# Performance work log

Measured on AMD Instinct MI355X. Metric: run time of the kernel, lower is better.

Reference implementation:

```python
import math
import jax, jax.numpy as jnp
import numpy as np

T, B, E, H = 2048, 1, 2048, 32
HD = E // H          # head_dim = 64
HALF = HD // 2       # rotary half = 32
SCALE_LENGTH = 1024


def duplicate_interleave(m):
    # [S, HALF] -> [S, HD], each column duplicated adjacently
    return jnp.repeat(m, 2, axis=-1)


def rotate_every_two(x):
    # x: [BH, S, HD]
    x1 = x[:, :, ::2]
    x2 = x[:, :, 1::2]
    return jnp.stack((-x2, x1), axis=-1).reshape(x.shape)


def apply_rotary_pos_emb(x, sin, cos, scale):
    # sin/cos/scale: [S, HALF]; x: [BH, S, HD]
    sin2 = duplicate_interleave(sin * scale)
    cos2 = duplicate_interleave(cos * scale)
    return x * cos2 + rotate_every_two(x) * sin2


def setup_inputs() -> dict:
    key = jax.random.key(0)
    ks = jax.random.split(key, 8)
    std = 0.02
    query = jax.random.normal(ks[0], (T, B, E), jnp.float32)
    key_t = jax.random.normal(ks[1], (T, B, E), jnp.float32)
    value = jax.random.normal(ks[2], (T, B, E), jnp.float32)
    Wq = jax.random.normal(ks[3], (E, E), jnp.float32) * std
    Wk = jax.random.normal(ks[4], (E, E), jnp.float32) * std
    Wv = jax.random.normal(ks[5], (E, E), jnp.float32) * std
    Wo = jax.random.normal(ks[6], (E, E), jnp.float32) * std
    bq = jnp.zeros((E,), jnp.float32)
    bk = jnp.zeros((E,), jnp.float32)
    bv = jnp.zeros((E,), jnp.float32)
    bo = jnp.zeros((E,), jnp.float32)
    # XPos-style rotary tables
    pos = jnp.arange(T, dtype=jnp.float32)
    inv_freq = 1.0 / (10000.0 ** (jnp.arange(HALF, dtype=jnp.float32) / HALF))
    ang = pos[:, None] * inv_freq[None, :]          # [T, HALF]
    sin = jnp.sin(ang)
    cos = jnp.cos(ang)
    scale_base = 512.0
    dim_scale = (jnp.arange(0, HD, 2, dtype=jnp.float32) + 0.4 * HD) / (1.4 * HD)
    xscale = dim_scale[None, :] ** (pos[:, None] / scale_base)  # [T, HALF]
    # causal additive mask
    attn_mask = jnp.where(jnp.triu(jnp.ones((T, T), bool), k=1), -1e9, 0.0).astype(jnp.float32)
    return {"query": query, "key": key_t, "value": value,
            "Wq": Wq, "bq": bq, "Wk": Wk, "bk": bk, "Wv": Wv, "bv": bv,
            "Wo": Wo, "bo": bo, "sin": sin, "cos": cos, "xscale": xscale,
            "attn_mask": attn_mask, "scale_length": SCALE_LENGTH}


def reference(query, key, value, Wq, bq, Wk, bk, Wv, bv, Wo, bo,
              sin, cos, xscale, attn_mask, scale_length):
    tgt_len, bsz, embed_dim = query.shape
    scaling = HD ** -0.5

    def proj(x, W, b):
        y = x @ W.T + b                                # [T, B, E]
        return y.reshape(tgt_len, bsz * H, HD).transpose(1, 0, 2)  # [BH, T, HD]

    q = proj(query, Wq, bq)
    k = proj(key, Wk, bk)
    v = proj(value, Wv, bv)

    # self-attention XPos rotary: k scaled by 1/xscale, q by xscale (last q_len rows)
    k = apply_rotary_pos_emb(k, sin, cos, 1.0 / xscale)
    q = apply_rotary_pos_emb(q, sin[-tgt_len:], cos[-tgt_len:], xscale[-tgt_len:])

    src_len = k.shape[1]
    if src_len > scale_length:
        pos_k = jnp.arange(src_len - tgt_len, src_len, dtype=jnp.float32)
        scale_attention = jnp.maximum(1.0, jnp.log(pos_k) / math.log(scale_length))
        q = q * scale_attention[None, :, None]

    q = q * scaling
    attn_weights = jnp.einsum('btd,bsd->bts', q, k)      # [BH, T, S]
    attn_weights = attn_weights + attn_mask[None, :, :]
    attn_weights = jax.nn.softmax(attn_weights.astype(jnp.float32), axis=-1
                                  ).astype(q.dtype)
    attn = jnp.einsum('bts,bsd->btd', attn_weights, v)   # [BH, T, HD]
    attn = attn.transpose(1, 0, 2).reshape(tgt_len, bsz, embed_dim)
    attn = attn @ Wo.T + bo
    return attn
```

## Files before the change

### kernel.cpp

```cpp
#include <hip/hip_runtime.h>
#include <hip/hip_bf16.h>
#include <math.h>

#define T_LEN 2048
#define EMB   2048
#define NH    32
#define HD    64
#define HALF  32

typedef __attribute__((ext_vector_type(8))) short short8v;
typedef __attribute__((ext_vector_type(4))) float floatx4;

__device__ inline void gload_lds16(const void* g, void* l) {
    __builtin_amdgcn_global_load_lds(
        (const __attribute__((address_space(1))) unsigned int*)g,
        (__attribute__((address_space(3))) unsigned int*)l,
        16, 0, 0);
}

__device__ inline ushort f2bf(float x) {
    union { float f; unsigned u; } c; c.f = x;
    const unsigned r = c.u + 0x7FFFu + ((c.u >> 16) & 1u);
    return (ushort)(r >> 16);
}

#define BARRIER() do { asm volatile("" ::: "memory"); \
    __builtin_amdgcn_s_barrier(); asm volatile("" ::: "memory"); } while (0)
#define VMW4() asm volatile("s_waitcnt vmcnt(4)" ::: "memory")

__global__ __launch_bounds__(256) void conv_all(
    const float* __restrict__ s0, const float* __restrict__ s1,
    const float* __restrict__ s2, const float* __restrict__ s3,
    const float* __restrict__ s4, const float* __restrict__ s5,
    const float* __restrict__ s6, ushort* __restrict__ dst)
{
    const int idx = blockIdx.x * 256 + threadIdx.x;
    const int t = idx >> 19;
    const int r = (idx & 524287) * 8;
    const float* in = t == 0 ? s0 : t == 1 ? s1 : t == 2 ? s2 : t == 3 ? s3
                    : t == 4 ? s4 : t == 5 ? s5 : s6;
    const float4 v0 = *reinterpret_cast<const float4*>(&in[r]);
    const float4 v1 = *reinterpret_cast<const float4*>(&in[r + 4]);
    ushort o[8];
    o[0] = f2bf(v0.x); o[1] = f2bf(v0.y); o[2] = f2bf(v0.z); o[3] = f2bf(v0.w);
    o[4] = f2bf(v1.x); o[5] = f2bf(v1.y); o[6] = f2bf(v1.z); o[7] = f2bf(v1.w);
    *reinterpret_cast<uint4*>(&dst[(size_t)t * 4194304 + r]) =
        *reinterpret_cast<const uint4*>(o);
}

__global__ __launch_bounds__(256) void rot_tables(
    const float* __restrict__ sinp, const float* __restrict__ cosp,
    const float* __restrict__ xscale,
    float2* __restrict__ qt, float2* __restrict__ kt)
{
    const int idx = blockIdx.x * 256 + threadIdx.x;
    const int t = idx >> 5;
    const float s = sinp[idx], c = cosp[idx], xs = xscale[idx];
    float sa = 1.f;
    if (t >= 2) {
        const float lv = __logf((float)t) * 0.14426950408889634f;
        sa = lv > 1.f ? lv : 1.f;
    }
    const float qs = xs * sa * 0.125f * 1.4426950408889634f;
    qt[idx] = make_float2(c * qs, s * qs);
    const float ks = 1.f / xs;
    kt[idx] = make_float2(c * ks, s * ks);
}

#define QBM 256
#define QBN 256

#define STAGE_A(tau, h) do {                                                   \
    const int _tc = ((tau) & 31) * 64;                                         \
    _Pragma("unroll") for (int _i = 0; _i < 2; ++_i) {                         \
        gload_lds16(&Ap[(size_t)(bm + (h) * 128 + wid * 16 + _i * 8 + rl) * 2048 + _tc + csw], \
                    &lds[((tau) & 1) * 16384 + (h) * 8192 + (wid * 16 + _i * 8) * 64]); \
    } } while (0)

#define STAGE_B(tau, h) do {                                                   \
    const int _tc = ((tau) & 31) * 64;                                         \
    _Pragma("unroll") for (int _i = 0; _i < 2; ++_i) {                         \
        gload_lds16(&Bp[(size_t)(bn + (h) * 128 + wid * 16 + _i * 8 + rl) * 2048 + _tc + csw], \
                    &lds[32768 + ((tau) & 1) * 16384 + (h) * 8192 + (wid * 16 + _i * 8) * 64]); \
    } } while (0)

#define PH(slot, mp, VMWSTMT, ...) do {                                        \
    if ((mp) == 0) {                                                           \
        _Pragma("unroll") for (int n = 0; n < 4; ++n) {                        \
            bf[n][0] = ldB(slot, n, 0);                                        \
            bf[n][1] = ldB(slot, n, 1);                                        \
        }                                                                      \
    }                                                                          \
    af[0][0] = ldA(slot, (mp) * 2, 0);     af[0][1] = ldA(slot, (mp) * 2, 1);  \
    af[1][0] = ldA(slot, (mp) * 2 + 1, 0); af[1][1] = ldA(slot, (mp) * 2 + 1, 1); \
    __VA_ARGS__;                                                               \
    BARRIER();                                                                 \
    __builtin_amdgcn_s_setprio(1);                                             \
    _Pragma("unroll") for (int mm = 0; mm < 2; ++mm)                           \
    _Pragma("unroll") for (int n = 0; n < 4; ++n)                              \
    _Pragma("unroll") for (int kk = 0; kk < 2; ++kk)                           \
        acc[(mp) * 2 + mm][n] = __builtin_amdgcn_mfma_f32_16x16x32_bf16(       \
            af[mm][kk], bf[n][kk], acc[(mp) * 2 + mm][n], 0, 0, 0);            \
    __builtin_amdgcn_s_setprio(0);                                             \
    VMWSTMT;                                                                   \
    BARRIER();                                                                 \
} while (0)

__global__ __launch_bounds__(512, 2) void gemm_qkv8(
    const ushort* __restrict__ Astack,
    const ushort* __restrict__ Wstack,
    const float* __restrict__ bq, const float* __restrict__ bk,
    const float* __restrict__ bv,
    ushort* __restrict__ outQ, ushort* __restrict__ outK,
    ushort* __restrict__ outVt,
    const float2* __restrict__ qtab, const float2* __restrict__ ktab)
{
    __shared__ ushort lds[65536];
    const int tid  = threadIdx.x;
    const int lane = tid & 63;
    const int wid  = tid >> 6;

    const int b   = blockIdx.x + blockIdx.y * 24;
    const int xcd = b & 7;
    const int idx = b >> 3;
    const int bx  = xcd * 3 + (idx >> 3);
    const int by  = idx & 7;
    const int which = bx >> 3;
    const int bn  = (bx & 7) * QBN;
    const int bm  = by * QBM;
    const ushort* Ap = Astack + (size_t)which * 4194304;
    const ushort* Bp = Wstack + (size_t)which * 4194304;

    const int rl  = lane >> 3;
    const int csw = (((lane & 7) ^ ((lane >> 3) & 7)) * 8);
    const int lm  = lane & 15;
    const int lg  = lane >> 4;
    const char* ldsb = reinterpret_cast<const char*>(lds);

    auto ldA = [&](int slot, int m, int kk) -> short8v {
        const int row = m * 16 + lm;
        const int off = (slot * 16384 + (wid >> 2) * 8192) * 2 + row * 128
                      + (((kk * 4 + lg) ^ (row & 7)) * 16);
        return *reinterpret_cast<const short8v*>(ldsb + off);
    };
    auto ldB = [&](int slot, int n, int kk) -> short8v {
        const int row = (wid & 1) * 64 + n * 16 + lm;
        const int off = (32768 + slot * 16384 + ((wid & 3) >> 1) * 8192) * 2
                      + row * 128 + (((kk * 4 + lg) ^ (row & 7)) * 16);
        return *reinterpret_cast<const short8v*>(ldsb + off);
    };

    floatx4 acc[8][4] = {};
    short8v bf[4][2];
    short8v af[2][2];

    STAGE_A(0, 0); STAGE_A(0, 1);
    STAGE_B(0, 0); STAGE_B(0, 1);
    STAGE_B(1, 0); STAGE_B(1, 1);
    VMW4();
    BARRIER();

    for (int i = 0; i < 16; ++i) {
        const int t = 2 * i;
        PH(0, 0, (void)0, STAGE_A(t + 1, 0));
        PH(0, 1, (void)0, STAGE_A(t + 1, 1));
        PH(0, 2, (void)0, STAGE_B(t + 2, 0));
        PH(0, 3, VMW4(),  STAGE_B(t + 2, 1));
        PH(1, 0, (void)0, STAGE_A(t + 2, 0));
        PH(1, 1, (void)0, STAGE_A(t + 2, 1));
        PH(1, 2, (void)0, STAGE_B(t + 3, 0));
        PH(1, 3, VMW4(),  STAGE_B(t + 3, 1));
    }
    asm volatile("s_waitcnt vmcnt(0)" ::: "memory");

    const float* bias = which == 0 ? bq : which == 1 ? bk : bv;
    const float2* tbl = which == 0 ? qtab : ktab;
    #pragma unroll
    for (int m = 0; m < 8; ++m) {
        #pragma unroll
        for (int n = 0; n < 4; ++n) {
            const int col = bn + (wid & 3) * 64 + n * 16 + lm;
            const float bz = bias[col];
            const int row0 = bm + (wid >> 2) * 128 + m * 16 + lg * 4;
            if (which == 2) {
                ushort o4[4];
                #pragma unroll
                for (int j = 0; j < 4; ++j)
                    o4[j] = f2bf(acc[m][n][j] + bz);
                *reinterpret_cast<uint2*>(&outVt[(size_t)col * T_LEN + row0]) =
                    *reinterpret_cast<const uint2*>(o4);
            } else {
                ushort* O = which == 0 ? outQ : outK;
                const int p = (col & 63) >> 1;
                const bool even = (col & 1) == 0;
                #pragma unroll
                for (int j = 0; j < 4; ++j) {
                    const int row = row0 + j;
                    const float v = acc[m][n][j] + bz;
                    const float pv = __shfl_xor(v, 1);
                    const float2 cs = tbl[row * HALF + p];
                    const float outv = even ? v * cs.x - pv * cs.y
                                            : v * cs.x + pv * cs.y;
                    O[(size_t)row * EMB + col] = f2bf(outv);
                }
            }
        }
    }
}

#define GBM 128
#define GBN 128
#define GBK 64

__global__ __launch_bounds__(256) void gemm_out(
    const ushort* __restrict__ A,
    const ushort* __restrict__ B,
    const float* __restrict__ bias,
    float* __restrict__ C)
{
    __shared__ ushort As[GBM * GBK];
    __shared__ ushort Bs[GBN * GBK];
    const int tid  = threadIdx.x;
    const int lane = tid & 63;
    const int wid  = tid >> 6;
    const int bm = blockIdx.y * GBM;
    const int bn = blockIdx.x * GBN;
    const int wr = (wid >> 1) * 64;
    const int wc = (wid & 1) * 64;

    floatx4 acc[4][4] = {};

    const int lrow  = lane >> 3;
    const int lcolb = (lane & 7) * 8;

    for (int k0 = 0; k0 < EMB; k0 += GBK) {
        #pragma unroll
        for (int c = 0; c < 4; ++c) {
            const int chunk = wid * 4 + c;
            const int row = chunk * 8 + lrow;
            gload_lds16(&A[(size_t)(bm + row) * EMB + k0 + lcolb], &As[chunk * 512]);
            gload_lds16(&B[(size_t)(bn + row) * EMB + k0 + lcolb], &Bs[chunk * 512]);
        }
        __syncthreads();
        #pragma unroll
        for (int kk = 0; kk < 2; ++kk) {
            short8v a[4], b[4];
            #pragma unroll
            for (int m = 0; m < 4; ++m)
                a[m] = *reinterpret_cast<const short8v*>(
                    &As[(wr + m * 16 + (lane & 15)) * GBK + kk * 32 + (lane >> 4) * 8]);
            #pragma unroll
            for (int n = 0; n < 4; ++n)
                b[n] = *reinterpret_cast<const short8v*>(
                    &Bs[(wc + n * 16 + (lane & 15)) * GBK + kk * 32 + (lane >> 4) * 8]);
            #pragma unroll
            for (int m = 0; m < 4; ++m)
                #pragma unroll
                for (int n = 0; n < 4; ++n)
                    acc[m][n] = __builtin_amdgcn_mfma_f32_16x16x32_bf16(
                        a[m], b[n], acc[m][n], 0, 0, 0);
        }
        __syncthreads();
    }

    const int cr = (lane >> 4) * 4;
    const int cc = lane & 15;
    #pragma unroll
    for (int m = 0; m < 4; ++m) {
        #pragma unroll
        for (int n = 0; n < 4; ++n) {
            const int col = bn + wc + n * 16 + cc;
            const float bz = bias[col];
            #pragma unroll
            for (int j = 0; j < 4; ++j) {
                const int row = bm + wr + m * 16 + cr + j;
                C[(size_t)row * EMB + col] = acc[m][n][j] + bz;
            }
        }
    }
}

__global__ __launch_bounds__(256) void flash_attn_mfma(
    const ushort* __restrict__ Qb,
    const ushort* __restrict__ Kb,
    const ushort* __restrict__ Vt,
    ushort* __restrict__ Ob)
{
    __shared__ ushort Ks[2][64 * 64];
    __shared__ ushort Vs[2][64 * 64];
    __shared__ ushort Ps[4][16 * 64];

    const int h   = blockIdx.x;
    const int qb  = (T_LEN / 64 - 1) - blockIdx.y;
    const int tid = threadIdx.x;
    const int lane = tid & 63;
    const int wid  = tid >> 6;
    const int qrow_w = qb * 64 + wid * 16;
    const int lm = lane & 15;
    const int lg = lane >> 4;

    short8v qf[2];
    {
        const ushort* qp = &Qb[(size_t)(qrow_w + lm) * EMB + h * HD + lg * 8];
        qf[0] = *reinterpret_cast<const short8v*>(qp);
        qf[1] = *reinterpret_cast<const short8v*>(qp + 32);
    }

    floatx4 oacc[4] = {};
    float m = -1e30f, l = 0.f;

    const int srow = lane >> 3;
    const int schk = lane & 7;

    {
        #pragma unroll
        for (int i = 0; i < 2; ++i) {
            const int slot = wid * 2 + i;
            const int row  = slot * 8 + srow;
            const int cswz = (schk ^ (row & 7)) * 8;
            gload_lds16(&Kb[(size_t)row * EMB + h * HD + cswz], &Ks[0][slot * 512]);
            gload_lds16(&Vt[(size_t)(h * HD + row) * T_LEN + cswz], &Vs[0][slot * 512]);
        }
    }
    __syncthreads();

    for (int kb = 0; kb <= qb; ++kb) {
        const int cur = kb & 1;
        if (kb < qb) {
            const int nkb = kb + 1;
            #pragma unroll
            for (int i = 0; i < 2; ++i) {
                const int slot = wid * 2 + i;
                const int row  = slot * 8 + srow;
                const int cswz = (schk ^ (row & 7)) * 8;
                gload_lds16(&Kb[(size_t)(nkb * 64 + row) * EMB + h * HD + cswz],
                            &Ks[cur ^ 1][slot * 512]);
                gload_lds16(&Vt[(size_t)(h * HD + row) * T_LEN + nkb * 64 + cswz],
                            &Vs[cur ^ 1][slot * 512]);
            }
        }

        float sv[16];
        #pragma unroll
        for (int t = 0; t < 4; ++t) {
            floatx4 sacc = {};
            const int srow_l = t * 16 + lm;
            const char* krow = reinterpret_cast<const char*>(Ks[cur]) + srow_l * 128;
            const int swz = (srow_l & 7) << 4;
            #pragma unroll
            for (int kk = 0; kk < 2; ++kk) {
                const int cb = (kk * 64 + lg * 16) ^ swz;
                short8v kf = *reinterpret_cast<const short8v*>(krow + cb);
                sacc = __builtin_amdgcn_mfma_f32_16x16x32_bf16(kf, qf[kk], sacc, 0, 0, 0);
            }
            sv[t * 4 + 0] = sacc[0]; sv[t * 4 + 1] = sacc[1];
            sv[t * 4 + 2] = sacc[2]; sv[t * 4 + 3] = sacc[3];
        }

        const int qg = qrow_w + lm;
        if (kb == qb) {
            #pragma unroll
            for (int t = 0; t < 4; ++t)
                #pragma unroll
                for (int r = 0; r < 4; ++r) {
                    const int sg = kb * 64 + t * 16 + lg * 4 + r;
                    if (sg > qg) sv[t * 4 + r] = -1e30f;
                }
        }

        float mx = sv[0];
        #pragma unroll
        for (int i = 1; i < 16; ++i) mx = fmaxf(mx, sv[i]);
        mx = fmaxf(mx, __shfl_xor(mx, 16));
        mx = fmaxf(mx, __shfl_xor(mx, 32));
        float corr = 1.f;
        if (!__all(mx - m <= 11.544f)) {
            const float mnew = fmaxf(m, mx);
            corr = exp2f(m - mnew);
            m = mnew;
            float corr4[4];
            #pragma unroll
            for (int r = 0; r < 4; ++r)
                corr4[r] = __shfl(corr, lg * 4 + r);
            #pragma unroll
            for (int td = 0; td < 4; ++td)
                #pragma unroll
                for (int r = 0; r < 4; ++r)
                    oacc[td][r] *= corr4[r];
        }
        float ps = 0.f;
        unsigned pw[8];
        #pragma unroll
        for (int i = 0; i < 8; ++i) {
            const float p0 = exp2f(sv[2 * i + 0] - m);
            const float p1 = exp2f(sv[2 * i + 1] - m);
            ps += p0 + p1;
            const __hip_bfloat162 h2 = __float22bfloat162_rn(make_float2(p0, p1));
            pw[i] = *reinterpret_cast<const unsigned*>(&h2);
        }
        ps += __shfl_xor(ps, 16);
        ps += __shfl_xor(ps, 32);
        l = l * corr + ps;

        {
            char* pbase = reinterpret_cast<char*>(&Ps[wid][0]) + lm * 128;
            const int swz = (lm & 7) << 4;
            #pragma unroll
            for (int t = 0; t < 4; ++t) {
                uint2 w;
                w.x = pw[2 * t + 0];
                w.y = pw[2 * t + 1];
                const int cb = (t * 32 + lg * 8) ^ swz;
                *reinterpret_cast<uint2*>(pbase + cb) = w;
            }
        }

        const char* pwave = reinterpret_cast<const char*>(&Ps[wid][0]);
        #pragma unroll
        for (int kk = 0; kk < 2; ++kk) {
            const int acb = (kk * 64 + lg * 16) ^ ((lm & 7) << 4);
            short8v pa = *reinterpret_cast<const short8v*>(pwave + lm * 128 + acb);
            #pragma unroll
            for (int td = 0; td < 4; ++td) {
                const int d = td * 16 + lm;
                const int bcb = (kk * 64 + lg * 16) ^ ((d & 7) << 4);
                short8v vb = *reinterpret_cast<const short8v*>(
                    reinterpret_cast<const char*>(Vs[cur]) + d * 128 + bcb);
                oacc[td] = __builtin_amdgcn_mfma_f32_16x16x32_bf16(pa, vb, oacc[td], 0, 0, 0);
            }
        }

        __syncthreads();
    }

    float invl[4];
    #pragma unroll
    for (int r = 0; r < 4; ++r)
        invl[r] = 1.f / __shfl(l, lg * 4 + r);
    #pragma unroll
    for (int td = 0; td < 4; ++td) {
        #pragma unroll
        for (int r = 0; r < 4; ++r) {
            const int trow = qrow_w + lg * 4 + r;
            const int col  = h * HD + td * 16 + lm;
            Ob[(size_t)trow * EMB + col] = f2bf(oacc[td][r] * invl[r]);
        }
    }
}

extern "C" void kernel_launch(void* const* d_in, const int* in_sizes, int n_in,
                              void* d_out, int out_size, void* d_ws, size_t ws_size,
                              hipStream_t stream) {
    const float* query = (const float*)d_in[0];
    const float* key   = (const float*)d_in[1];
    const float* value = (const float*)d_in[2];
    const float* Wq = (const float*)d_in[3];
    const float* bq = (const float*)d_in[4];
    const float* Wk = (const float*)d_in[5];
    const float* bk = (const float*)d_in[6];
    const float* Wv = (const float*)d_in[7];
    const float* bv = (const float*)d_in[8];
    const float* Wo = (const float*)d_in[9];
    const float* bo = (const float*)d_in[10];
    const float* sinp   = (const float*)d_in[11];
    const float* cosp   = (const float*)d_in[12];
    const float* xscale = (const float*)d_in[13];
    float* out = (float*)d_out;

    const size_t MB = 1024 * 1024;
    char* ws = (char*)d_ws;
    ushort* bWqkv = (ushort*)(ws + 0 * MB);
    ushort* bWo   = (ushort*)(ws + 24 * MB);
    ushort* bAqkv = (ushort*)(ws + 32 * MB);
    ushort* bQ  = (ushort*)(ws + 56 * MB);
    ushort* bK  = (ushort*)(ws + 64 * MB);
    ushort* bVt = (ushort*)(ws + 72 * MB);
    ushort* bAo = (ushort*)(ws + 80 * MB);
    float2* qtab = (float2*)(ws + 88 * MB);
    float2* ktab = (float2*)(ws + 88 * MB + 512 * 1024);

    conv_all<<<7 * 524288 / 256, 256, 0, stream>>>(
        Wq, Wk, Wv, Wo, query, key, value, bWqkv);
    rot_tables<<<T_LEN * HALF / 256, 256, 0, stream>>>(
        sinp, cosp, xscale, qtab, ktab);

    dim3 gQKV(24, 8);
    gemm_qkv8<<<gQKV, 512, 0, stream>>>(bAqkv, bWqkv, bq, bk, bv,
                                        bQ, bK, bVt, qtab, ktab);

    dim3 gFlash(NH, T_LEN / 64);
    flash_attn_mfma<<<gFlash, 256, 0, stream>>>(bQ, bK, bVt, bAo);

    dim3 gGemm(EMB / GBN, T_LEN / GBM);
    gemm_out<<<gGemm, 256, 0, stream>>>(bAo, bWo, bo, out);
}
```

Before: 183.3 us.

## Process 128 query rows per flash-attention block, 32 per wave

Each flash-attention workgroup now covers 128 query rows instead of 64, with each wave handling two 16-row sub-tiles that share the K/V tiles held in LDS. This halves the K/V global-to-LDS traffic per query row and reuses each V fragment load for two MFMAs. Waves skip key blocks that lie entirely past their causal limit, but still take part in the barriers. In exchange the grid is half as large (512 blocks), register pressure rises from the doubled accumulators and Q fragments, and load balance across waves at the diagonal gets worse.

```diff
diff --git a/kernel.cpp b/kernel.cpp
--- a/kernel.cpp
+++ b/kernel.cpp
@@ -288,162 +288,185 @@
 {
     __shared__ ushort Ks[2][64 * 64];
     __shared__ ushort Vs[2][64 * 64];
-    __shared__ ushort Ps[4][16 * 64];
+    __shared__ ushort Ps[4][32 * 64];
 
     const int h   = blockIdx.x;
-    const int qb  = (T_LEN / 64 - 1) - blockIdx.y;
+    const int qb  = (T_LEN / 128 - 1) - blockIdx.y;
     const int tid = threadIdx.x;
     const int lane = tid & 63;
     const int wid  = tid >> 6;
-    const int qrow_w = qb * 64 + wid * 16;
+    const int qrow_w = qb * 128 + wid * 32;
     const int lm = lane & 15;
     const int lg = lane >> 4;
 
-    short8v qf[2];
-    {
-        const ushort* qp = &Qb[(size_t)(qrow_w + lm) * EMB + h * HD + lg * 8];
-        qf[0] = *reinterpret_cast<const short8v*>(qp);
-        qf[1] = *reinterpret_cast<const short8v*>(qp + 32);
-    }
-
-    floatx4 oacc[4] = {};
-    float m = -1e30f, l = 0.f;
+    short8v qf[2][2];
+    #pragma unroll
+    for (int s = 0; s < 2; ++s) {
+        const ushort* qp = &Qb[(size_t)(qrow_w + s * 16 + lm) * EMB + h * HD + lg * 8];
+        qf[s][0] = *reinterpret_cast<const short8v*>(qp);
+        qf[s][1] = *reinterpret_cast<const short8v*>(qp + 32);
+    }
+
+    floatx4 oacc[2][4] = {};
+    float m0 = -1e30f, m1 = -1e30f;
+    float l0 = 0.f, l1 = 0.f;
 
     const int srow = lane >> 3;
     const int schk = lane & 7;
-
-    {
-        #pragma unroll
-        for (int i = 0; i < 2; ++i) {
-            const int slot = wid * 2 + i;
-            const int row  = slot * 8 + srow;
-            const int cswz = (schk ^ (row & 7)) * 8;
-            gload_lds16(&Kb[(size_t)row * EMB + h * HD + cswz], &Ks[0][slot * 512]);
-            gload_lds16(&Vt[(size_t)(h * HD + row) * T_LEN + cswz], &Vs[0][slot * 512]);
-        }
+    const int nkb = 2 * qb + 2;
+
+    #pragma unroll
+    for (int i = 0; i < 2; ++i) {
+        const int slot = wid * 2 + i;
+        const int row  = slot * 8 + srow;
+        const int cswz = (schk ^ (row & 7)) * 8;
+        gload_lds16(&Kb[(size_t)row * EMB + h * HD + cswz], &Ks[0][slot * 512]);
+        gload_lds16(&Vt[(size_t)(h * HD + row) * T_LEN + cswz], &Vs[0][slot * 512]);
     }
     __syncthreads();
 
-    for (int kb = 0; kb <= qb; ++kb) {
+    for (int kb = 0; kb < nkb; ++kb) {
         const int cur = kb & 1;
-        if (kb < qb) {
-            const int nkb = kb + 1;
+        if (kb + 1 < nkb) {
+            const int nk = kb + 1;
             #pragma unroll
             for (int i = 0; i < 2; ++i) {
                 const int slot = wid * 2 + i;
                 const int row  = slot * 8 + srow;
                 const int cswz = (schk ^ (row & 7)) * 8;
-                gload_lds16(&Kb[(size_t)(nkb * 64 + row) * EMB + h * HD + cswz],
+                gload_lds16(&Kb[(size_t)(nk * 64 + row) * EMB + h * HD + cswz],
                             &Ks[cur ^ 1][slot * 512]);
-                gload_lds16(&Vt[(size_t)(h * HD + row) * T_LEN + nkb * 64 + cswz],
+                gload_lds16(&Vt[(size_t)(h * HD + row) * T_LEN + nk * 64 + cswz],
                             &Vs[cur ^ 1][slot * 512]);
             }
         }
 
-        float sv[16];
+        if (kb * 64 <= qrow_w + 31) {
+            const bool diag = (kb * 64 + 63 > qrow_w);
+
+            #pragma unroll
+            for (int s = 0; s < 2; ++s) {
+                float& m = s ? m1 : m0;
+                float& l = s ? l1 : l0;
+
+                float sv[16];
+                #pragma unroll
+                for (int t = 0; t < 4; ++t) {
+                    floatx4 sacc = {};
+                    const int srow_l = t * 16 + lm;
+                    const char* krow = reinterpret_cast<const char*>(Ks[cur]) + srow_l * 128;
+                    const int swz = (srow_l & 7) << 4;
+                    #pragma unroll
+                    for (int kk = 0; kk < 2; ++kk) {
+                        const int cb = (kk * 64 + lg * 16) ^ swz;
+                        short8v kf = *reinterpret_cast<const short8v*>(krow + cb);
+                        sacc = __builtin_amdgcn_mfma_f32_16x16x32_bf16(
+                            kf, qf[s][kk], sacc, 0, 0, 0);
+                    }
+                    sv[t * 4 + 0] = sacc[0]; sv[t * 4 + 1] = sacc[1];
+                    sv[t * 4 + 2] = sacc[2]; sv[t * 4 + 3] = sacc[3];
+                }
+
+                const int qg = qrow_w + s * 16 + lm;
+                if (diag) {
+                    #pragma unroll
+                    for (int t = 0; t < 4; ++t)
+                        #pragma unroll
+                        for (int r = 0; r < 4; ++r) {
+                            const int sg = kb * 64 + t * 16 + lg * 4 + r;
+                            if (sg > qg) sv[t * 4 + r] = -1e30f;
+                        }
+                }
+
+                float mx = sv[0];
+                #pragma unroll
+                for (int i = 1; i < 16; ++i) mx = fmaxf(mx, sv[i]);
+                mx = fmaxf(mx, __shfl_xor(mx, 16));
+                mx = fmaxf(mx, __shfl_xor(mx, 32));
+                float corr = 1.f;
+                if (!__all(mx - m <= 11.544f)) {
+                    const float mnew = fmaxf(m, mx);
+                    corr = exp2f(m - mnew);
+                    m = mnew;
+                    float corr4[4];
+                    #pragma unroll
+                    for (int r = 0; r < 4; ++r)
+                        corr4[r] = __shfl(corr, lg * 4 + r);
+                    #pragma unroll
+                    for (int td = 0; td < 4; ++td)
+                        #pragma unroll
+                        for (int r = 0; r < 4; ++r)
+                            oacc[s][td][r] *= corr4[r];
+                }
+                float ps = 0.f;
+                unsigned pw[8];
+                #pragma unroll
+                for (int i = 0; i < 8; ++i) {
+                    const float p0 = exp2f(sv[2 * i + 0] - m);
+                    const float p1 = exp2f(sv[2 * i + 1] - m);
+                    ps += p0 + p1;
+                    const __hip_bfloat162 h2 = __float22bfloat162_rn(make_float2(p0, p1));
+                    pw[i] = *reinterpret_cast<const unsigned*>(&h2);
+                }
+                ps += __shfl_xor(ps, 16);
+                ps += __shfl_xor(ps, 32);
+                l = l * corr + ps;
+
+                {
+                    char* pbase = reinterpret_cast<char*>(&Ps[wid][0])
+                                + (s * 16 + lm) * 128;
+                    const int swz = (lm & 7) << 4;
+                    #pragma unroll
+                    for (int t = 0; t < 4; ++t) {
+                        uint2 w;
+                        w.x = pw[2 * t + 0];
+                        w.y = pw[2 * t + 1];
+                        const int cb = (t * 32 + lg * 8) ^ swz;
+                        *reinterpret_cast<uint2*>(pbase + cb) = w;
+                    }
+                }
+            }
+
+            const char* pwave = reinterpret_cast<const char*>(&Ps[wid][0]);
+            #pragma unroll
+            for (int kk = 0; kk < 2; ++kk) {
+                const int acb = (kk * 64 + lg * 16) ^ ((lm & 7) << 4);
+                short8v pa0 = *reinterpret_cast<const short8v*>(
+                    pwave + (0 * 16 + lm) * 128 + acb);
+                short8v pa1 = *reinterpret_cast<const short8v*>(
+                    pwave + (1 * 16 + lm) * 128 + acb);
+                #pragma unroll
+                for (int td = 0; td < 4; ++td) {
+                    const int d = td * 16 + lm;
+                    const int bcb = (kk * 64 + lg * 16) ^ ((d & 7) << 4);
+                    short8v vb = *reinterpret_cast<const short8v*>(
+                        reinterpret_cast<const char*>(Vs[cur]) + d * 128 + bcb);
+                    oacc[0][td] = __builtin_amdgcn_mfma_f32_16x16x32_bf16(
+                        pa0, vb, oacc[0][td], 0, 0, 0);
+                    oacc[1][td] = __builtin_amdgcn_mfma_f32_16x16x32_bf16(
+                        pa1, vb, oacc[1][td], 0, 0, 0);
+                }
+            }
+        }
+
+        __syncthreads();
+    }
+
+    #pragma unroll
+    for (int s = 0; s < 2; ++s) {
+        const float lsrc = s ? l1 : l0;
+        float invl[4];
         #pragma unroll
-        for (int t = 0; t < 4; ++t) {
-            floatx4 sacc = {};
-            const int srow_l = t * 16 + lm;
-            const char* krow = reinterpret_cast<const char*>(Ks[cur]) + srow_l * 128;
-            const int swz = (srow_l & 7) << 4;
-            #pragma unroll
-            for (int kk = 0; kk < 2; ++kk) {
-                const int cb = (kk * 64 + lg * 16) ^ swz;
-                short8v kf = *reinterpret_cast<const short8v*>(krow + cb);
-                sacc = __builtin_amdgcn_mfma_f32_16x16x32_bf16(kf, qf[kk], sacc, 0, 0, 0);
+        for (int r = 0; r < 4; ++r)
+            invl[r] = 1.f / __shfl(lsrc, lg * 4 + r);
+        #pragma unroll
+        for (int td = 0; td < 4; ++td) {
+            #pragma unroll
+            for (int r = 0; r < 4; ++r) {
+                const int trow = qrow_w + s * 16 + lg * 4 + r;
+                const int col  = h * HD + td * 16 + lm;
+                Ob[(size_t)trow * EMB + col] = f2bf(oacc[s][td][r] * invl[r]);
             }
-            sv[t * 4 + 0] = sacc[0]; sv[t * 4 + 1] = sacc[1];
-            sv[t * 4 + 2] = sacc[2]; sv[t * 4 + 3] = sacc[3];
-        }
-
-        const int qg = qrow_w + lm;
-        if (kb == qb) {
-            #pragma unroll
-            for (int t = 0; t < 4; ++t)
-                #pragma unroll
-                for (int r = 0; r < 4; ++r) {
-                    const int sg = kb * 64 + t * 16 + lg * 4 + r;
-                    if (sg > qg) sv[t * 4 + r] = -1e30f;
-                }
-        }
-
-        float mx = sv[0];
-        #pragma unroll
-        for (int i = 1; i < 16; ++i) mx = fmaxf(mx, sv[i]);
-        mx = fmaxf(mx, __shfl_xor(mx, 16));
-        mx = fmaxf(mx, __shfl_xor(mx, 32));
-        float corr = 1.f;
-        if (!__all(mx - m <= 11.544f)) {
-            const float mnew = fmaxf(m, mx);
-            corr = exp2f(m - mnew);
-            m = mnew;
-            float corr4[4];
-            #pragma unroll
-            for (int r = 0; r < 4; ++r)
-                corr4[r] = __shfl(corr, lg * 4 + r);
-            #pragma unroll
-            for (int td = 0; td < 4; ++td)
-                #pragma unroll
-                for (int r = 0; r < 4; ++r)
-                    oacc[td][r] *= corr4[r];
-        }
-        float ps = 0.f;
-        unsigned pw[8];
-        #pragma unroll
-        for (int i = 0; i < 8; ++i) {
-            const float p0 = exp2f(sv[2 * i + 0] - m);
-            const float p1 = exp2f(sv[2 * i + 1] - m);
-            ps += p0 + p1;
-            const __hip_bfloat162 h2 = __float22bfloat162_rn(make_float2(p0, p1));
-            pw[i] = *reinterpret_cast<const unsigned*>(&h2);
-        }
-        ps += __shfl_xor(ps, 16);
-        ps += __shfl_xor(ps, 32);
-        l = l * corr + ps;
-
-        {
-            char* pbase = reinterpret_cast<char*>(&Ps[wid][0]) + lm * 128;
-            const int swz = (lm & 7) << 4;
-            #pragma unroll
-            for (int t = 0; t < 4; ++t) {
-                uint2 w;
-                w.x = pw[2 * t + 0];
-                w.y = pw[2 * t + 1];
-                const int cb = (t * 32 + lg * 8) ^ swz;
-                *reinterpret_cast<uint2*>(pbase + cb) = w;
-            }
-        }
-
-        const char* pwave = reinterpret_cast<const char*>(&Ps[wid][0]);
-        #pragma unroll
-        for (int kk = 0; kk < 2; ++kk) {
-            const int acb = (kk * 64 + lg * 16) ^ ((lm & 7) << 4);
-            short8v pa = *reinterpret_cast<const short8v*>(pwave + lm * 128 + acb);
-            #pragma unroll
-            for (int td = 0; td < 4; ++td) {
-                const int d = td * 16 + lm;
-                const int bcb = (kk * 64 + lg * 16) ^ ((d & 7) << 4);
-                short8v vb = *reinterpret_cast<const short8v*>(
-                    reinterpret_cast<const char*>(Vs[cur]) + d * 128 + bcb);
-                oacc[td] = __builtin_amdgcn_mfma_f32_16x16x32_bf16(pa, vb, oacc[td], 0, 0, 0);
-            }
-        }
-
-        __syncthreads();
-    }
-
-    float invl[4];
-    #pragma unroll
-    for (int r = 0; r < 4; ++r)
-        invl[r] = 1.f / __shfl(l, lg * 4 + r);
-    #pragma unroll
-    for (int td = 0; td < 4; ++td) {
-        #pragma unroll
-        for (int r = 0; r < 4; ++r) {
-            const int trow = qrow_w + lg * 4 + r;
-            const int col  = h * HD + td * 16 + lm;
-            Ob[(size_t)trow * EMB + col] = f2bf(oacc[td][r] * invl[r]);
         }
     }
 }
@@ -488,7 +511,7 @@
     gemm_qkv8<<<gQKV, 512, 0, stream>>>(bAqkv, bWqkv, bq, bk, bv,
                                         bQ, bK, bVt, qtab, ktab);
 
-    dim3 gFlash(NH, T_LEN / 64);
+    dim3 gFlash(NH, T_LEN / 128);
     flash_attn_mfma<<<gFlash, 256, 0, stream>>>(bQ, bK, bVt, bAo);
 
     dim3 gGemm(EMB / GBN, T_LEN / GBM);
```

Result: slower. 206.3 us (+12.5%).
